# Kernel optimization log

Hardware: AMD Instinct MI355X
Metric: run time of the kernel (lower is better)

Reference implementation:

```python
import jax, jax.numpy as jnp
import numpy as np

CH = 64          # channels
OC = 64          # out_channels
B, H, W = 8, 128, 128
NCA_C = CH + OC  # 128, NCA state channels
K = 3            # kernel_size
DILS = (1, 2, 4, 8)
HID = 64         # NCA update hidden
EPS = 1e-5


def setup_inputs() -> dict:
    key = jax.random.key(0)
    ks = jax.random.split(key, 16)
    def n(k, shape, s=0.02):
        return jax.random.normal(k, shape, jnp.float32) * s
    return {
        "x": jax.random.normal(ks[0], (B, H, W, CH), jnp.float32),
        "c": jax.random.normal(ks[1], (B, OC), jnp.float32),
        # Attention params
        "Wq": n(ks[2], (CH, OC)), "bq": jnp.zeros((OC,), jnp.float32),
        "Wk": n(ks[3], (OC, OC)), "bk": jnp.zeros((OC,), jnp.float32),
        "Wv": n(ks[4], (OC, OC)), "bv": jnp.zeros((OC,), jnp.float32),
        "Wo": n(ks[5], (OC, OC)), "bo": jnp.zeros((OC,), jnp.float32),
        "ln_g": jnp.ones((OC,), jnp.float32), "ln_b": jnp.zeros((OC,), jnp.float32),
        # NCA depthwise perception kernels, one per dilation: [4, NCA_C, 1, K, K]
        "pk": n(ks[6], (len(DILS), NCA_C, 1, K, K), 0.1),
        # NCA update MLP
        "W1": n(ks[7], ((1 + len(DILS)) * NCA_C, HID)), "b1": jnp.zeros((HID,), jnp.float32),
        "W2": n(ks[8], (HID, CH)), "b2": jnp.zeros((CH,), jnp.float32),
    }


def _layernorm(z, g, b):
    m = jnp.mean(z, axis=-1, keepdims=True)
    v = jnp.var(z, axis=-1, keepdims=True)
    return (z - m) / jnp.sqrt(v + EPS) * g + b


def _forward(x, c, Wq, bq, Wk, bk, Wv, bv, Wo, bo, ln_g, ln_b, pk, W1, b1, W2, b2):
    b_, h_, w_, _ = x.shape
    # ---- Attention(x, c): single-key softmax pooling over H*W ----
    q = x.reshape(b_, h_ * w_, CH) @ Wq + bq              # [B, HW, OC]
    k = c @ Wk + bk                                        # [B, OC]
    v = c @ Wv + bv                                        # [B, OC]
    scores = jnp.einsum('bno,bo->bn', q, k) * (OC ** -0.5)  # [B, HW]
    attn = jax.nn.softmax(scores, axis=1)                  # softmax over spatial dim
    attended = jnp.einsum('bn,bo->bo', attn, v)            # weighted pool (weights sum to 1)
    a = _layernorm(attended @ Wo + bo + c, ln_g, ln_b)     # out_proj + residual + LN
    c2 = c + a                                             # outer residual in NCAAttention

    # ---- concat broadcast context -> NCA state [B,H,W,NCA_C] ----
    c_exp = jnp.broadcast_to(c2[:, None, None, :], (b_, h_, w_, OC))
    xc = jnp.concatenate([x, c_exp], axis=-1)

    # ---- NCA perception: depthwise dilated convs (SAME padding) ----
    xp = jnp.transpose(xc, (0, 3, 1, 2))                   # NCHW
    feats = [xc]
    for i, d in enumerate(DILS):
        pad = d * (K // 2)
        p = jax.lax.conv_general_dilated(
            xp, pk[i], window_strides=(1, 1),
            padding=[(pad, pad), (pad, pad)], rhs_dilation=(d, d),
            dimension_numbers=('NCHW', 'OIHW', 'NCHW'),
            feature_group_count=NCA_C)
        feats.append(jnp.transpose(p, (0, 2, 3, 1)))
    upd_in = jnp.concatenate(feats, axis=-1)               # [B,H,W,5*NCA_C]

    # ---- NCA update MLP: Linear -> (Dropout=id) -> GELU -> Linear ----
    hidden = jax.nn.gelu(upd_in @ W1 + b1, approximate=False)
    y = hidden @ W2 + b2                                   # [B,H,W,CH]
    # NCA.out_channels (64) != NCA.channels (128) -> no residual add
    return y, c2


def reference(x, c, Wq, bq, Wk, bk, Wv, bv, Wo, bo, ln_g, ln_b, pk, W1, b1, W2, b2):
    return _forward(x, c, Wq, bq, Wk, bk, Wv, bv, Wo, bo, ln_g, ln_b, pk, W1, b1, W2, b2)
```

## Files before the change

### kernel.cpp

```cpp
#include <hip/hip_runtime.h>
#include <hip/hip_bf16.h>
#include <math.h>


typedef float  f32x4 __attribute__((ext_vector_type(4)));
typedef short  s16x8 __attribute__((ext_vector_type(8)));
typedef long   i64;

static __device__ __forceinline__ unsigned short f2bf(float f) {
    __hip_bfloat16 h = __float2bfloat16(f);
    unsigned short u; __builtin_memcpy(&u, &h, 2); return u;
}
static __device__ __forceinline__ unsigned pk4fp8(float f0, float f1, float f2, float f3) {
    int v = 0;
    v = __builtin_amdgcn_cvt_pk_fp8_f32(f0, f1, v, false);
    v = __builtin_amdgcn_cvt_pk_fp8_f32(f2, f3, v, true);
    return (unsigned)v;
}

#define XROW   2304
#define XPLANE 331776
#define XBATCH 1327104
#define USCALE 256.0f

__global__ void prepA(const float* __restrict__ x, const float* __restrict__ c,
                      const float* __restrict__ Wv, const float* __restrict__ bv,
                      const float* __restrict__ Wo, const float* __restrict__ bo,
                      const float* __restrict__ lng, const float* __restrict__ lnb,
                      unsigned char* __restrict__ xp, float* __restrict__ c2f,
                      float* __restrict__ outc2)
{
    const int blk = blockIdx.x, tid = threadIdx.x;
    if (blk < 512) {
        int i = blk*256 + tid;
        int xc = i & 127, y = (i >> 7) & 127, b = i >> 14;
        const float* src = x + (size_t)i*64;
        unsigned char* dstb = xp + ((size_t)b*4*144 + (y+8))*XROW + (xc+8)*16;
        #pragma unroll
        for (int p = 0; p < 4; ++p) {
            float4 f0 = *(const float4*)(src + p*16 + 0);
            float4 f1 = *(const float4*)(src + p*16 + 4);
            float4 f2 = *(const float4*)(src + p*16 + 8);
            float4 f3 = *(const float4*)(src + p*16 + 12);
            uint4 o;
            o.x = pk4fp8(f0.x, f0.y, f0.z, f0.w);
            o.y = pk4fp8(f1.x, f1.y, f1.z, f1.w);
            o.z = pk4fp8(f2.x, f2.y, f2.z, f2.w);
            o.w = pk4fp8(f3.x, f3.y, f3.z, f3.w);
            *(uint4*)(dstb + (size_t)p*XPLANE) = o;
        }
    } else if (blk < 1056) {
        int idx = (blk - 512)*256 + tid;
        int bp = idx / 4352;
        int r  = idx - bp*4352;
        int yy, xx;
        if (r < 2304) { int ry = r / 144; xx = r - ry*144; yy = (ry < 8) ? ry : 128 + ry; }
        else { int r2 = r - 2304; yy = 8 + (r2 >> 4); int xi = r2 & 15; xx = (xi < 8) ? xi : 128 + xi; }
        *(uint4*)(xp + ((size_t)bp*144 + yy)*XROW + xx*16) = make_uint4(0,0,0,0);
    } else {
        const int b = blk - 1056;
        __shared__ float sc[64], sv[64];
        const int j = tid;
        if (j < 64) sc[j] = c[b*64 + j];
        __syncthreads();
        if (j < 64) {
            float v = bv[j];
            for (int i = 0; i < 64; ++i) v += sc[i]*Wv[i*64 + j];
            sv[j] = v;
        }
        __syncthreads();
        if (j < 64) {
            float t = bo[j] + sc[j];
            for (int i = 0; i < 64; ++i) t += sv[i]*Wo[i*64 + j];
            float s = t;
            for (int o = 32; o > 0; o >>= 1) s += __shfl_xor(s, o);
            float m = s * (1.f/64.f);
            float dq = (t - m)*(t - m);
            for (int o = 32; o > 0; o >>= 1) dq += __shfl_xor(dq, o);
            float a = (t - m) / sqrtf(dq*(1.f/64.f) + 1e-5f) * lng[j] + lnb[j];
            float c2 = sc[j] + a;
            c2f[b*64 + j] = c2;
            outc2[b*64 + j] = c2;
        }
    }
}

__global__ void prepB(const float* __restrict__ pk, const float* __restrict__ W1,
                      const float* __restrict__ W2, const float* __restrict__ b1,
                      const float* __restrict__ c2f,
                      unsigned char* __restrict__ Uf, unsigned short* __restrict__ W2s,
                      float* __restrict__ V, float* __restrict__ hcp)
{
    const int blk = blockIdx.x, tid = threadIdx.x;
    if (blk < 66) {
        int idx = blk*256 + tid;
        int lane = idx & 63, nt = (idx >> 6) & 3, kc2 = (idx >> 8) & 1, pos = idx >> 9;
        int n  = nt*16 + (lane & 15);
        int k0 = kc2*32 + (lane >> 4)*8;
        static constexpr int DI[33] = {3,3,3, 2,2,2, 1,1,1, 0,0,0, -1, 0,0, 1,1, 2,2, 3,3,
                                       0,0,0, 1,1,1, 2,2,2, 3,3,3};
        static constexpr int TT[33] = {0,1,2, 0,1,2, 0,1,2, 0,1,2, 4, 3,5, 3,5, 3,5, 3,5,
                                       6,7,8, 6,7,8, 6,7,8, 6,7,8};
        int di = DI[pos], t = TT[pos];
        float vv[8];
        #pragma unroll
        for (int j = 0; j < 8; ++j) {
            int ch = k0 + j;
            float v;
            if (di < 0) {
                v = W1[ch*64 + n];
                for (int dd = 0; dd < 4; ++dd)
                    v += pk[(dd*128 + ch)*9 + 4] * W1[((1+dd)*128 + ch)*64 + n];
            } else {
                v = pk[(di*128 + ch)*9 + t] * W1[((1+di)*128 + ch)*64 + n];
            }
            vv[j] = v * USCALE;
        }
        uint2 o;
        o.x = pk4fp8(vv[0], vv[1], vv[2], vv[3]);
        o.y = pk4fp8(vv[4], vv[5], vv[6], vv[7]);
        *(uint2*)(Uf + (size_t)idx*8) = o;
    } else if (blk < 68) {
        int idx = (blk-66)*256 + tid;
        int lane = idx & 63, nt = (idx >> 6) & 3, kc2 = (idx >> 8) & 1;
        int n  = nt*16 + (lane & 15);
        int k0 = kc2*32 + (lane >> 4)*8;
        unsigned short e[8];
        #pragma unroll
        for (int j = 0; j < 8; ++j) e[j] = f2bf(W2[(k0+j)*64 + n]);
        uint4 o;
        o.x = (unsigned)e[0] | ((unsigned)e[1] << 16);
        o.y = (unsigned)e[2] | ((unsigned)e[3] << 16);
        o.z = (unsigned)e[4] | ((unsigned)e[5] << 16);
        o.w = (unsigned)e[6] | ((unsigned)e[7] << 16);
        *(uint4*)(W2s + (size_t)idx*8) = o;
    } else if (blk < 140) {
        int idx = (blk-68)*256 + tid;
        int n = idx & 63, q = idx >> 6;
        int p = q % 36, b = q / 36;
        int di = p/9, t = p%9;
        float s = 0.f;
        for (int j = 0; j < 64; ++j)
            s += c2f[b*64 + j] * pk[(di*128 + 64 + j)*9 + t] * W1[((1+di)*128 + 64 + j)*64 + n];
        V[(size_t)q*64 + n] = s;
    } else {
        for (int it = tid; it < 512; it += 256) {
            int b = it >> 6, n = it & 63;
            float s = b1[n];
            for (int j = 0; j < 64; ++j) s += c2f[b*64 + j]*W1[(64 + j)*64 + n];
            hcp[it] = s;
        }
    }
}

#define HID_S 72

__global__ __launch_bounds__(256) void nca_main(
    const unsigned char* __restrict__ xp,
    const unsigned char* __restrict__ U,
    const unsigned short* __restrict__ W2s,
    const float* __restrict__ V,
    const float* __restrict__ hcp,
    const float* __restrict__ b2,
    float* __restrict__ out)
{
    __shared__ unsigned short hid[256*HID_S];
    __shared__ float V_l[36*64];
    __shared__ float Cx_l[16*64];
    __shared__ float Cy_l[2*64];
    __shared__ float hc2_l[64];

    const int tid = threadIdx.x;
    const int blk = blockIdx.x;
    const int b  = blk & 7;
    const int y0 = (blk >> 3) * 2;

    {
        const float4* Vg = (const float4*)(V + (size_t)b*2304);
        for (int i = tid; i < 576; i += 256) ((float4*)V_l)[i] = Vg[i];
    }
    __syncthreads();
    for (int it = tid; it < 1024; it += 256) {
        int xi = it >> 6, n = it & 63;
        int xx = xi < 8 ? xi : 112 + xi;
        float s = 0.f;
        #pragma unroll
        for (int di = 0; di < 4; ++di) {
            int d = 1 << di;
            int dxo = (xx < d) ? 0 : ((xx >= 128 - d) ? 2 : -1);
            if (dxo >= 0) {
                s += V_l[(di*9 + 0*3 + dxo)*64 + n];
                s += V_l[(di*9 + 1*3 + dxo)*64 + n];
                s += V_l[(di*9 + 2*3 + dxo)*64 + n];
            }
        }
        Cx_l[it] = s;
    }
    for (int it = tid; it < 128; it += 256) {
        int r = it >> 6, n = it & 63;
        int yy = y0 + r;
        float s = 0.f;
        #pragma unroll
        for (int di = 0; di < 4; ++di) {
            int d = 1 << di;
            int dyo = (yy < d) ? 0 : ((yy >= 128 - d) ? 2 : -1);
            if (dyo >= 0) {
                s += V_l[(di*9 + dyo*3 + 0)*64 + n];
                s += V_l[(di*9 + dyo*3 + 1)*64 + n];
                s += V_l[(di*9 + dyo*3 + 2)*64 + n];
            }
        }
        Cy_l[it] = s;
    }
    if (tid < 64) {
        float s = hcp[b*64 + tid];
        for (int p = 0; p < 36; ++p) s += V_l[p*64 + tid];
        hc2_l[tid] = s;
    }
    __syncthreads();

    const int lane = tid & 63;
    const int w    = tid >> 6;
    const int y    = y0 + (w >> 1);
    const int xw   = (w & 1) * 64;
    const int ln15 = lane & 15;
    const int oct  = lane >> 4;

    const unsigned char* base0 = xp + (size_t)b*XBATCH + (size_t)(oct >> 1)*XPLANE
                               + (size_t)(y + 8)*XROW + (size_t)(xw + ln15 + 8)*16
                               + (oct & 1)*8;

    f32x4 acc[4][4];
    #pragma unroll
    for (int mt = 0; mt < 4; ++mt)
        #pragma unroll
        for (int nt = 0; nt < 4; ++nt) {
            acc[mt][nt][0] = 0.f; acc[mt][nt][1] = 0.f;
            acc[mt][nt][2] = 0.f; acc[mt][nt][3] = 0.f;
        }

    static constexpr int OFF[33] = {
        (-8*144-8)*16, (-8*144)*16, (-8*144+8)*16,
        (-4*144-4)*16, (-4*144)*16, (-4*144+4)*16,
        (-2*144-2)*16, (-2*144)*16, (-2*144+2)*16,
        (-1*144-1)*16, (-1*144)*16, (-1*144+1)*16,
        0,
        -1*16, 1*16, -2*16, 2*16, -4*16, 4*16, -8*16, 8*16,
        ( 1*144-1)*16, ( 1*144)*16, ( 1*144+1)*16,
        ( 2*144-2)*16, ( 2*144)*16, ( 2*144+2)*16,
        ( 4*144-4)*16, ( 4*144)*16, ( 4*144+4)*16,
        ( 8*144-8)*16, ( 8*144)*16, ( 8*144+8)*16
    };

    i64 avc[2][4];
    #pragma unroll
    for (int kc2 = 0; kc2 < 2; ++kc2)
        #pragma unroll
        for (int mt = 0; mt < 4; ++mt)
            avc[kc2][mt] = *(const i64*)(base0 + OFF[0] + kc2*(2*XPLANE) + mt*256);

    #pragma unroll 1
    for (int pos = 0; pos < 33; ++pos) {
        i64 avn[2][4];
        if (pos < 32) {
            const unsigned char* rp = base0 + OFF[pos + 1];
            #pragma unroll
            for (int kc2 = 0; kc2 < 2; ++kc2)
                #pragma unroll
                for (int mt = 0; mt < 4; ++mt)
                    avn[kc2][mt] = *(const i64*)(rp + kc2*(2*XPLANE) + mt*256);
        }
        const unsigned char* Up = U + (size_t)pos*4096 + lane*8;
        #pragma unroll
        for (int kc2 = 0; kc2 < 2; ++kc2) {
            #pragma unroll
            for (int nt = 0; nt < 4; ++nt) {
                i64 bf = *(const i64*)(Up + kc2*2048 + nt*512);
                #pragma unroll
                for (int mt = 0; mt < 4; ++mt)
                    acc[mt][nt] = __builtin_amdgcn_mfma_f32_16x16x32_fp8_fp8(avc[kc2][mt], bf, acc[mt][nt], 0, 0, 0);
            }
        }
        #pragma unroll
        for (int kc2 = 0; kc2 < 2; ++kc2)
            #pragma unroll
            for (int mt = 0; mt < 4; ++mt)
                avc[kc2][mt] = avn[kc2][mt];
    }

    const bool yedge = (y < 8) || (y >= 120);
    #pragma unroll
    for (int mt = 0; mt < 4; ++mt) {
        #pragma unroll
        for (int nt = 0; nt < 4; ++nt) {
            const int n = nt*16 + ln15;
            const float hcv = hc2_l[n];
            const float cyv = yedge ? Cy_l[(w >> 1)*64 + n] : 0.f;
            #pragma unroll
            for (int r = 0; r < 4; ++r) {
                int m = oct*4 + r;
                int x = xw + mt*16 + m;
                float h = acc[mt][nt][r]*(1.0f/USCALE) + hcv - cyv;
                if (x < 8 || x >= 120) {
                    int xi = (x < 8) ? x : (x - 112);
                    h -= Cx_l[xi*64 + n];
                    if (yedge) {
                        #pragma unroll
                        for (int di = 0; di < 4; ++di) {
                            int d = 1 << di;
                            int dyo = (y < d) ? 0 : ((y >= 128 - d) ? 2 : -1);
                            int dxo = (x < d) ? 0 : ((x >= 128 - d) ? 2 : -1);
                            if (dyo >= 0 && dxo >= 0)
                                h += V_l[(di*9 + dyo*3 + dxo)*64 + n];
                        }
                    }
                }
                float u = 0.7978845608028654f * (h + 0.044715f*h*h*h);
                float g = h / (1.f + __expf(-2.f*u));
                hid[(w*64 + mt*16 + m)*HID_S + n] = f2bf(g);
            }
        }
    }

    f32x4 acc2[4][4];
    #pragma unroll
    for (int mt = 0; mt < 4; ++mt)
        #pragma unroll
        for (int nt = 0; nt < 4; ++nt) {
            acc2[mt][nt][0] = 0.f; acc2[mt][nt][1] = 0.f;
            acc2[mt][nt][2] = 0.f; acc2[mt][nt][3] = 0.f;
        }
    #pragma unroll
    for (int kc2 = 0; kc2 < 2; ++kc2) {
        s16x8 a2[4];
        #pragma unroll
        for (int mt = 0; mt < 4; ++mt)
            a2[mt] = *(const s16x8*)&hid[(w*64 + mt*16 + ln15)*HID_S + kc2*32 + oct*8];
        #pragma unroll
        for (int nt = 0; nt < 4; ++nt) {
            s16x8 bf = *(const s16x8*)(W2s + ((size_t)(kc2*4 + nt)*64 + lane)*8);
            #pragma unroll
            for (int mt = 0; mt < 4; ++mt)
                acc2[mt][nt] = __builtin_amdgcn_mfma_f32_16x16x32_bf16(a2[mt], bf, acc2[mt][nt], 0, 0, 0);
        }
    }

    float* ob = out + ((size_t)(b*128 + y))*128*64;
    #pragma unroll
    for (int nt = 0; nt < 4; ++nt) {
        const float b2v = b2[nt*16 + ln15];
        #pragma unroll
        for (int mt = 0; mt < 4; ++mt) {
            #pragma unroll
            for (int r = 0; r < 4; ++r) {
                int x = xw + mt*16 + oct*4 + r;
                ob[(size_t)x*64 + nt*16 + ln15] = acc2[mt][nt][r] + b2v;
            }
        }
    }
}

extern "C" void kernel_launch(void* const* d_in, const int* in_sizes, int n_in,
                              void* d_out, int out_size, void* d_ws, size_t ws_size,
                              hipStream_t stream) {
    const float* x   = (const float*)d_in[0];
    const float* c   = (const float*)d_in[1];
    const float* Wv  = (const float*)d_in[6];
    const float* bv  = (const float*)d_in[7];
    const float* Wo  = (const float*)d_in[8];
    const float* bo  = (const float*)d_in[9];
    const float* lng = (const float*)d_in[10];
    const float* lnb = (const float*)d_in[11];
    const float* pk  = (const float*)d_in[12];
    const float* W1  = (const float*)d_in[13];
    const float* b1  = (const float*)d_in[14];
    const float* W2  = (const float*)d_in[15];
    const float* b2  = (const float*)d_in[16];
    float* out = (float*)d_out;

    char* w = (char*)d_ws;
    unsigned char*  xpb = (unsigned char*)(w);
    unsigned char*  Uf  = (unsigned char*)(w + 10616832);
    unsigned short* W2s = (unsigned short*)(w + 10752000);
    float*          V   = (float*)         (w + 10760192);
    float*          hcp = (float*)         (w + 10833920);
    float*          c2f = (float*)         (w + 10835968);

    prepA<<<1064, 256, 0, stream>>>(x, c, Wv, bv, Wo, bo, lng, lnb, xpb, c2f, out + 8388608);
    prepB<<<141, 256, 0, stream>>>(pk, W1, W2, b1, c2f, Uf, W2s, V, hcp);
    nca_main<<<512, 256, 0, stream>>>(xpb, Uf, W2s, V, hcp, b2, out);
}
```

Measured before the change: 167.8 us.

## Interleave fp8 padded input per pixel and use 16-byte A/B fragment loads

The padded fp8 copy of x is reordered from four 16-channel planes into one 64-byte record per pixel, with channels interleaved so each lane can fetch both k-chunks of its MFMA A fragment in a single 16-byte load. The packed weight tensor U is laid out the same way, and its fragments are now prefetched one position ahead alongside the activations. The prep kernels are regrouped so the small attention/LayerNorm kernel runs first and everything else runs in one larger launch, which keeps the number of launches unchanged. The aim is fewer, wider global loads and less scattered traffic in the main loop, at the cost of more live registers for the double-buffered fragments.

```diff
diff --git a/kernel.cpp b/kernel.cpp
--- a/kernel.cpp
+++ b/kernel.cpp
@@ -5,7 +5,7 @@
 
 typedef float  f32x4 __attribute__((ext_vector_type(4)));
 typedef short  s16x8 __attribute__((ext_vector_type(8)));
-typedef long   i64;
+typedef long   i64x2 __attribute__((ext_vector_type(2)));
 
 static __device__ __forceinline__ unsigned short f2bf(float f) {
     __hip_bfloat16 h = __float2bfloat16(f);
@@ -18,110 +18,103 @@
     return (unsigned)v;
 }
 
-#define XROW   2304
-#define XPLANE 331776
+#define XROWB  9216
 #define XBATCH 1327104
 #define USCALE 256.0f
 
-__global__ void prepA(const float* __restrict__ x, const float* __restrict__ c,
+__global__ void prep1(const float* __restrict__ c,
                       const float* __restrict__ Wv, const float* __restrict__ bv,
                       const float* __restrict__ Wo, const float* __restrict__ bo,
                       const float* __restrict__ lng, const float* __restrict__ lnb,
-                      unsigned char* __restrict__ xp, float* __restrict__ c2f,
-                      float* __restrict__ outc2)
+                      float* __restrict__ c2f, float* __restrict__ outc2)
+{
+    const int b = blockIdx.x, j = threadIdx.x;
+    __shared__ float sc[64], sv[64];
+    float cj = c[b*64 + j];
+    sc[j] = cj; __syncthreads();
+    float v = bv[j];
+    for (int i = 0; i < 64; ++i) v += sc[i]*Wv[i*64 + j];
+    sv[j] = v; __syncthreads();
+    float t = bo[j] + cj;
+    for (int i = 0; i < 64; ++i) t += sv[i]*Wo[i*64 + j];
+    float s = t;
+    for (int o = 32; o > 0; o >>= 1) s += __shfl_xor(s, o);
+    float m = s * (1.f/64.f);
+    float dq = (t - m)*(t - m);
+    for (int o = 32; o > 0; o >>= 1) dq += __shfl_xor(dq, o);
+    float a = (t - m) / sqrtf(dq*(1.f/64.f) + 1e-5f) * lng[j] + lnb[j];
+    float c2 = cj + a;
+    c2f[b*64 + j] = c2;
+    outc2[b*64 + j] = c2;
+}
+
+__global__ void prep2(const float* __restrict__ x,  const float* __restrict__ pk,
+                      const float* __restrict__ W1, const float* __restrict__ W2,
+                      const float* __restrict__ b1, const float* __restrict__ c2f,
+                      unsigned char* __restrict__ xp, unsigned char* __restrict__ Uf,
+                      unsigned short* __restrict__ W2s,
+                      float* __restrict__ V, float* __restrict__ hcp)
 {
     const int blk = blockIdx.x, tid = threadIdx.x;
     if (blk < 512) {
         int i = blk*256 + tid;
         int xc = i & 127, y = (i >> 7) & 127, b = i >> 14;
         const float* src = x + (size_t)i*64;
-        unsigned char* dstb = xp + ((size_t)b*4*144 + (y+8))*XROW + (xc+8)*16;
-        #pragma unroll
-        for (int p = 0; p < 4; ++p) {
-            float4 f0 = *(const float4*)(src + p*16 + 0);
-            float4 f1 = *(const float4*)(src + p*16 + 4);
-            float4 f2 = *(const float4*)(src + p*16 + 8);
-            float4 f3 = *(const float4*)(src + p*16 + 12);
-            uint4 o;
-            o.x = pk4fp8(f0.x, f0.y, f0.z, f0.w);
-            o.y = pk4fp8(f1.x, f1.y, f1.z, f1.w);
-            o.z = pk4fp8(f2.x, f2.y, f2.z, f2.w);
-            o.w = pk4fp8(f3.x, f3.y, f3.z, f3.w);
-            *(uint4*)(dstb + (size_t)p*XPLANE) = o;
-        }
-    } else if (blk < 1056) {
+        float4 f[16];
+        #pragma unroll
+        for (int k = 0; k < 16; ++k) f[k] = *(const float4*)(src + k*4);
+        unsigned P[16];
+        #pragma unroll
+        for (int k = 0; k < 16; ++k) P[k] = pk4fp8(f[k].x, f[k].y, f[k].z, f[k].w);
+        unsigned char* d = xp + (size_t)b*XBATCH + (size_t)(y+8)*XROWB + (size_t)(xc+8)*64;
+        *(uint4*)(d +  0) = make_uint4(P[0], P[1], P[8],  P[9]);
+        *(uint4*)(d + 16) = make_uint4(P[2], P[3], P[10], P[11]);
+        *(uint4*)(d + 32) = make_uint4(P[4], P[5], P[12], P[13]);
+        *(uint4*)(d + 48) = make_uint4(P[6], P[7], P[14], P[15]);
+    } else if (blk < 648) {
         int idx = (blk - 512)*256 + tid;
-        int bp = idx / 4352;
-        int r  = idx - bp*4352;
+        int b = idx / 4352, r = idx - b*4352;
         int yy, xx;
         if (r < 2304) { int ry = r / 144; xx = r - ry*144; yy = (ry < 8) ? ry : 128 + ry; }
         else { int r2 = r - 2304; yy = 8 + (r2 >> 4); int xi = r2 & 15; xx = (xi < 8) ? xi : 128 + xi; }
-        *(uint4*)(xp + ((size_t)bp*144 + yy)*XROW + xx*16) = make_uint4(0,0,0,0);
-    } else {
-        const int b = blk - 1056;
-        __shared__ float sc[64], sv[64];
-        const int j = tid;
-        if (j < 64) sc[j] = c[b*64 + j];
-        __syncthreads();
-        if (j < 64) {
-            float v = bv[j];
-            for (int i = 0; i < 64; ++i) v += sc[i]*Wv[i*64 + j];
-            sv[j] = v;
-        }
-        __syncthreads();
-        if (j < 64) {
-            float t = bo[j] + sc[j];
-            for (int i = 0; i < 64; ++i) t += sv[i]*Wo[i*64 + j];
-            float s = t;
-            for (int o = 32; o > 0; o >>= 1) s += __shfl_xor(s, o);
-            float m = s * (1.f/64.f);
-            float dq = (t - m)*(t - m);
-            for (int o = 32; o > 0; o >>= 1) dq += __shfl_xor(dq, o);
-            float a = (t - m) / sqrtf(dq*(1.f/64.f) + 1e-5f) * lng[j] + lnb[j];
-            float c2 = sc[j] + a;
-            c2f[b*64 + j] = c2;
-            outc2[b*64 + j] = c2;
-        }
-    }
-}
-
-__global__ void prepB(const float* __restrict__ pk, const float* __restrict__ W1,
-                      const float* __restrict__ W2, const float* __restrict__ b1,
-                      const float* __restrict__ c2f,
-                      unsigned char* __restrict__ Uf, unsigned short* __restrict__ W2s,
-                      float* __restrict__ V, float* __restrict__ hcp)
-{
-    const int blk = blockIdx.x, tid = threadIdx.x;
-    if (blk < 66) {
-        int idx = blk*256 + tid;
-        int lane = idx & 63, nt = (idx >> 6) & 3, kc2 = (idx >> 8) & 1, pos = idx >> 9;
-        int n  = nt*16 + (lane & 15);
-        int k0 = kc2*32 + (lane >> 4)*8;
-        static constexpr int DI[33] = {3,3,3, 2,2,2, 1,1,1, 0,0,0, -1, 0,0, 1,1, 2,2, 3,3,
-                                       0,0,0, 1,1,1, 2,2,2, 3,3,3};
-        static constexpr int TT[33] = {0,1,2, 0,1,2, 0,1,2, 0,1,2, 4, 3,5, 3,5, 3,5, 3,5,
-                                       6,7,8, 6,7,8, 6,7,8, 6,7,8};
-        int di = DI[pos], t = TT[pos];
-        float vv[8];
-        #pragma unroll
-        for (int j = 0; j < 8; ++j) {
-            int ch = k0 + j;
-            float v;
-            if (di < 0) {
-                v = W1[ch*64 + n];
-                for (int dd = 0; dd < 4; ++dd)
-                    v += pk[(dd*128 + ch)*9 + 4] * W1[((1+dd)*128 + ch)*64 + n];
-            } else {
-                v = pk[(di*128 + ch)*9 + t] * W1[((1+di)*128 + ch)*64 + n];
-            }
-            vv[j] = v * USCALE;
-        }
-        uint2 o;
-        o.x = pk4fp8(vv[0], vv[1], vv[2], vv[3]);
-        o.y = pk4fp8(vv[4], vv[5], vv[6], vv[7]);
-        *(uint2*)(Uf + (size_t)idx*8) = o;
-    } else if (blk < 68) {
-        int idx = (blk-66)*256 + tid;
+        unsigned char* d = xp + (size_t)b*XBATCH + (size_t)yy*XROWB + (size_t)xx*64;
+        uint4 z = make_uint4(0,0,0,0);
+        *(uint4*)(d) = z; *(uint4*)(d+16) = z; *(uint4*)(d+32) = z; *(uint4*)(d+48) = z;
+    } else if (blk < 681) {
+        int idx = (blk - 648)*256 + tid;
+        if (idx < 8448) {
+            int lane = idx & 63, nt = (idx >> 6) & 3, pos = idx >> 8;
+            int n  = nt*16 + (lane & 15);
+            static constexpr int DI[33] = {3,3,3, 2,2,2, 1,1,1, 0,0,0, -1, 0,0, 1,1, 2,2, 3,3,
+                                           0,0,0, 1,1,1, 2,2,2, 3,3,3};
+            static constexpr int TT[33] = {0,1,2, 0,1,2, 0,1,2, 0,1,2, 4, 3,5, 3,5, 3,5, 3,5,
+                                           6,7,8, 6,7,8, 6,7,8, 6,7,8};
+            int di = DI[pos], t = TT[pos];
+            float vv[16];
+            #pragma unroll
+            for (int kc2 = 0; kc2 < 2; ++kc2)
+                #pragma unroll
+                for (int j = 0; j < 8; ++j) {
+                    int ch = kc2*32 + (lane >> 4)*8 + j;
+                    float v;
+                    if (di < 0) {
+                        v = W1[ch*64 + n];
+                        for (int dd = 0; dd < 4; ++dd)
+                            v += pk[(dd*128 + ch)*9 + 4] * W1[((1+dd)*128 + ch)*64 + n];
+                    } else {
+                        v = pk[(di*128 + ch)*9 + t] * W1[((1+di)*128 + ch)*64 + n];
+                    }
+                    vv[kc2*8 + j] = v * USCALE;
+                }
+            uint4 o;
+            o.x = pk4fp8(vv[0],  vv[1],  vv[2],  vv[3]);
+            o.y = pk4fp8(vv[4],  vv[5],  vv[6],  vv[7]);
+            o.z = pk4fp8(vv[8],  vv[9],  vv[10], vv[11]);
+            o.w = pk4fp8(vv[12], vv[13], vv[14], vv[15]);
+            *(uint4*)(Uf + (size_t)idx*16) = o;
+        }
+    } else if (blk < 683) {
+        int idx = (blk - 681)*256 + tid;
         int lane = idx & 63, nt = (idx >> 6) & 3, kc2 = (idx >> 8) & 1;
         int n  = nt*16 + (lane & 15);
         int k0 = kc2*32 + (lane >> 4)*8;
@@ -134,8 +127,8 @@
         o.z = (unsigned)e[4] | ((unsigned)e[5] << 16);
         o.w = (unsigned)e[6] | ((unsigned)e[7] << 16);
         *(uint4*)(W2s + (size_t)idx*8) = o;
-    } else if (blk < 140) {
-        int idx = (blk-68)*256 + tid;
+    } else if (blk < 755) {
+        int idx = (blk - 683)*256 + tid;
         int n = idx & 63, q = idx >> 6;
         int p = q % 36, b = q / 36;
         int di = p/9, t = p%9;
@@ -226,9 +219,9 @@
     const int ln15 = lane & 15;
     const int oct  = lane >> 4;
 
-    const unsigned char* base0 = xp + (size_t)b*XBATCH + (size_t)(oct >> 1)*XPLANE
-                               + (size_t)(y + 8)*XROW + (size_t)(xw + ln15 + 8)*16
-                               + (oct & 1)*8;
+    const unsigned char* abase = xp + (size_t)b*XBATCH + (size_t)(y + 8)*XROWB
+                               + (size_t)(xw + ln15 + 8)*64 + oct*16;
+    const unsigned char* ubase = U + (size_t)lane*16;
 
     f32x4 acc[4][4];
     #pragma unroll
@@ -240,52 +233,48 @@
         }
 
     static constexpr int OFF[33] = {
-        (-8*144-8)*16, (-8*144)*16, (-8*144+8)*16,
-        (-4*144-4)*16, (-4*144)*16, (-4*144+4)*16,
-        (-2*144-2)*16, (-2*144)*16, (-2*144+2)*16,
-        (-1*144-1)*16, (-1*144)*16, (-1*144+1)*16,
+        (-8*144-8)*64, (-8*144)*64, (-8*144+8)*64,
+        (-4*144-4)*64, (-4*144)*64, (-4*144+4)*64,
+        (-2*144-2)*64, (-2*144)*64, (-2*144+2)*64,
+        (-1*144-1)*64, (-1*144)*64, (-1*144+1)*64,
         0,
-        -1*16, 1*16, -2*16, 2*16, -4*16, 4*16, -8*16, 8*16,
-        ( 1*144-1)*16, ( 1*144)*16, ( 1*144+1)*16,
-        ( 2*144-2)*16, ( 2*144)*16, ( 2*144+2)*16,
-        ( 4*144-4)*16, ( 4*144)*16, ( 4*144+4)*16,
-        ( 8*144-8)*16, ( 8*144)*16, ( 8*144+8)*16
+        -64, 64, -128, 128, -256, 256, -512, 512,
+        ( 1*144-1)*64, ( 1*144)*64, ( 1*144+1)*64,
+        ( 2*144-2)*64, ( 2*144)*64, ( 2*144+2)*64,
+        ( 4*144-4)*64, ( 4*144)*64, ( 4*144+4)*64,
+        ( 8*144-8)*64, ( 8*144)*64, ( 8*144+8)*64
     };
 
-    i64 avc[2][4];
-    #pragma unroll
-    for (int kc2 = 0; kc2 < 2; ++kc2)
-        #pragma unroll
-        for (int mt = 0; mt < 4; ++mt)
-            avc[kc2][mt] = *(const i64*)(base0 + OFF[0] + kc2*(2*XPLANE) + mt*256);
+    i64x2 Ac[4], An[4], Bc[4], Bn[4];
+    #pragma unroll
+    for (int mt = 0; mt < 4; ++mt) Ac[mt] = *(const i64x2*)(abase + OFF[0] + mt*1024);
+    #pragma unroll
+    for (int nt = 0; nt < 4; ++nt) Bc[nt] = *(const i64x2*)(ubase + nt*1024);
 
     #pragma unroll 1
     for (int pos = 0; pos < 33; ++pos) {
-        i64 avn[2][4];
         if (pos < 32) {
-            const unsigned char* rp = base0 + OFF[pos + 1];
-            #pragma unroll
-            for (int kc2 = 0; kc2 < 2; ++kc2)
+            const unsigned char* rp = abase + OFF[pos + 1];
+            #pragma unroll
+            for (int mt = 0; mt < 4; ++mt) An[mt] = *(const i64x2*)(rp + mt*1024);
+            const unsigned char* up = ubase + (size_t)(pos + 1)*4096;
+            #pragma unroll
+            for (int nt = 0; nt < 4; ++nt) Bn[nt] = *(const i64x2*)(up + nt*1024);
+        }
+        #pragma unroll
+        for (int kc2 = 0; kc2 < 2; ++kc2) {
+            #pragma unroll
+            for (int nt = 0; nt < 4; ++nt) {
+                long bf = Bc[nt][kc2];
                 #pragma unroll
                 for (int mt = 0; mt < 4; ++mt)
-                    avn[kc2][mt] = *(const i64*)(rp + kc2*(2*XPLANE) + mt*256);
-        }
-        const unsigned char* Up = U + (size_t)pos*4096 + lane*8;
-        #pragma unroll
-        for (int kc2 = 0; kc2 < 2; ++kc2) {
-            #pragma unroll
-            for (int nt = 0; nt < 4; ++nt) {
-                i64 bf = *(const i64*)(Up + kc2*2048 + nt*512);
-                #pragma unroll
-                for (int mt = 0; mt < 4; ++mt)
-                    acc[mt][nt] = __builtin_amdgcn_mfma_f32_16x16x32_fp8_fp8(avc[kc2][mt], bf, acc[mt][nt], 0, 0, 0);
-            }
-        }
-        #pragma unroll
-        for (int kc2 = 0; kc2 < 2; ++kc2)
-            #pragma unroll
-            for (int mt = 0; mt < 4; ++mt)
-                avc[kc2][mt] = avn[kc2][mt];
+                    acc[mt][nt] = __builtin_amdgcn_mfma_f32_16x16x32_fp8_fp8(Ac[mt][kc2], bf, acc[mt][nt], 0, 0, 0);
+            }
+        }
+        #pragma unroll
+        for (int mt = 0; mt < 4; ++mt) Ac[mt] = An[mt];
+        #pragma unroll
+        for (int nt = 0; nt < 4; ++nt) Bc[nt] = Bn[nt];
     }
 
     const bool yedge = (y < 8) || (y >= 120);
@@ -386,7 +375,7 @@
     float*          hcp = (float*)         (w + 10833920);
     float*          c2f = (float*)         (w + 10835968);
 
-    prepA<<<1064, 256, 0, stream>>>(x, c, Wv, bv, Wo, bo, lng, lnb, xpb, c2f, out + 8388608);
-    prepB<<<141, 256, 0, stream>>>(pk, W1, W2, b1, c2f, Uf, W2s, V, hcp);
+    prep1<<<8, 64, 0, stream>>>(c, Wv, bv, Wo, bo, lng, lnb, c2f, out + 8388608);
+    prep2<<<757, 256, 0, stream>>>(x, pk, W1, W2, b1, c2f, xpb, Uf, W2s, V, hcp);
     nca_main<<<512, 256, 0, stream>>>(xpb, Uf, W2s, V, hcp, b2, out);
 }
```

After: 162.6 us. 1.03x faster.
